# Performance work log

Hardware: AMD Instinct MI355X
Metric: run time of the kernel (lower is better)

Reference implementation:

```python
import jax, jax.numpy as jnp
import numpy as np


def setup_inputs() -> dict:
    key = jax.random.key(0)
    ks = jax.random.split(key, 6)
    B, S, D, E = 4, 2048, 1024, 8
    H = 4 * D
    return {
        "x": jax.random.normal(ks[0], (B, S, D), dtype=jnp.float32),
        "logits": jax.random.normal(ks[1], (B, S, E), dtype=jnp.float32),
        "noise": jax.random.normal(ks[2], (B, S, E), dtype=jnp.float32),
        "W1": jax.random.normal(ks[3], (E, D, H), dtype=jnp.float32) * (1.0 / np.sqrt(D)),
        "b1": jnp.zeros((E, H), dtype=jnp.float32),
        "W2": jax.random.normal(ks[4], (E, H, D), dtype=jnp.float32) * (1.0 / np.sqrt(H)),
        "b2": jnp.zeros((E, D), dtype=jnp.float32),
        "top_k": 2,
    }


def reference(x, logits, noise, W1, b1, W2, b2, top_k):
    # NoisyTopkRouter_Cluster: noise scaled by softplus(logits), then sparse top-k softmax
    B, S, D = x.shape
    E = logits.shape[-1]
    noisy = logits + noise * jax.nn.softplus(logits)           # [B,S,E]
    _, topi = jax.lax.top_k(noisy, top_k)                      # [B,S,K]
    in_topk = jax.nn.one_hot(topi, E, dtype=jnp.bool_).any(-2)  # [B,S,E]
    sparse = jnp.where(in_topk, noisy, -jnp.inf)
    gates = jax.nn.softmax(sparse, axis=-1)                    # [B,S,E]; zero off top-k

    # SparseMoE combine: sum_e gate[:, e] * Expert_e(x). Gate is exactly 0 for
    # unselected experts, so dense-masked compute matches the gather/scatter loop.
    xf = x.reshape(-1, D)                                      # [T,D]
    gf = gates.reshape(-1, E).T                                # [E,T]

    def body(acc, params):
        w1, bb1, w2, bb2, g = params                           # g: [T]
        h = jax.nn.relu(xf @ w1 + bb1)                         # [T,4D]
        acc = acc + (h @ w2 + bb2) * g[:, None]
        return acc, None

    acc, _ = jax.lax.scan(body, jnp.zeros_like(xf), (W1, b1, W2, b2, gf))
    return acc.reshape(B, S, D)
```

## Files before the change

### kernel.cpp

```cpp
#include <hip/hip_runtime.h>
#include <cstdint>
#include <cstddef>

#define T_TOK 8192
#define E_NUM 8
#define D_DIM 1024
#define H_DIM 4096
#define MAXTILES 136
#define TILE 128
#define BK 32

typedef __attribute__((ext_vector_type(8))) short short8;
typedef __attribute__((ext_vector_type(4))) float f32x4;
typedef __attribute__((ext_vector_type(8))) unsigned short ushort8v;
typedef __attribute__((ext_vector_type(4))) unsigned short ushort4v;

__device__ __forceinline__ unsigned short f2b(float f) {
  unsigned int u = __float_as_uint(f);
  u += 0x7fffu + ((u >> 16) & 1u);
  return (unsigned short)(u >> 16);
}

__device__ __forceinline__ void async16(const void* g, void* l) {
  __builtin_amdgcn_global_load_lds((const __attribute__((address_space(1))) void*)g,
                                   (__attribute__((address_space(3))) void*)l, 16, 0, 0);
}

__global__ void router_kernel(const float* __restrict__ logits, const float* __restrict__ noise,
                              int* __restrict__ counts, int* __restrict__ ti, float* __restrict__ tg) {
  int tk = blockIdx.x * blockDim.x + threadIdx.x;
  if (tk >= T_TOK) return;
  float nz[E_NUM];
#pragma unroll
  for (int e = 0; e < E_NUM; ++e) {
    float l = logits[tk * E_NUM + e];
    float sp = fmaxf(l, 0.f) + log1pf(expf(-fabsf(l)));
    nz[e] = l + noise[tk * E_NUM + e] * sp;
  }
  int i1 = 0; float v1 = nz[0];
#pragma unroll
  for (int e = 1; e < E_NUM; ++e) if (nz[e] > v1) { v1 = nz[e]; i1 = e; }
  int i2 = -1; float v2 = -3.0e38f;
#pragma unroll
  for (int e = 0; e < E_NUM; ++e) if (e != i1 && nz[e] > v2) { v2 = nz[e]; i2 = e; }
  float ex = expf(v2 - v1);
  float g1 = 1.f / (1.f + ex);
  float g2 = ex / (1.f + ex);
  int s1 = atomicAdd(&counts[i1], 1);
  int s2 = atomicAdd(&counts[i2], 1);
  ti[tk*4+0] = i1; ti[tk*4+1] = s1; ti[tk*4+2] = i2; ti[tk*4+3] = s2;
  tg[tk*2+0] = g1; tg[tk*2+1] = g2;
}

__global__ void setup_kernel(const int* __restrict__ counts, int* __restrict__ offs,
                             int* __restrict__ tab) {
  int o = 0;
  for (int e = 0; e < E_NUM; ++e) { offs[e] = o; o += counts[e]; }
  offs[E_NUM] = o;
  int mt = 0;
  for (int e = 0; e < E_NUM; ++e)
    for (int m0 = 0; m0 < counts[e]; m0 += TILE) { tab[mt*2] = e; tab[mt*2+1] = m0; ++mt; }
  for (; mt < MAXTILES; ++mt) { tab[mt*2] = -1; tab[mt*2+1] = 0; }
}

__global__ void gather_kernel(const float* __restrict__ x, const int* __restrict__ ti,
                              const float* __restrict__ tg, const int* __restrict__ offs,
                              unsigned short* __restrict__ xg, int* __restrict__ stok,
                              float* __restrict__ sg) {
  const int tk = blockIdx.x, t = threadIdx.x;
  const int i1 = ti[tk*4+0], s1 = ti[tk*4+1], i2 = ti[tk*4+2], s2 = ti[tk*4+3];
  const int r1 = offs[i1] + s1, r2 = offs[i2] + s2;
  if (t == 0) {
    stok[r1] = tk; sg[r1] = tg[tk*2+0];
    stok[r2] = tk; sg[r2] = tg[tk*2+1];
  }
  const float4 v = *(const float4*)(x + (size_t)tk * D_DIM + t * 4);
  ushort4v bb; bb.x = f2b(v.x); bb.y = f2b(v.y); bb.z = f2b(v.z); bb.w = f2b(v.w);
  *(ushort4v*)(xg + (size_t)r1 * D_DIM + t * 4) = bb;
  *(ushort4v*)(xg + (size_t)r2 * D_DIM + t * 4) = bb;
}

__global__ void transpose_kernel(const float* __restrict__ W, unsigned short* __restrict__ Wt,
                                 int K, int N) {
  const int e = blockIdx.z;
  const float* We = W + (size_t)e * K * N;
  unsigned short* Wte = Wt + (size_t)e * K * N;
  __shared__ __align__(16) unsigned short tb[64 * 72];
  const int n0 = blockIdx.x * 64, k0 = blockIdx.y * 64;
  const int t = threadIdx.x;
  const int kr = t >> 4;
  const int c4 = (t & 15) * 4;
#pragma unroll
  for (int rr = 0; rr < 4; ++rr) {
    int k = kr + rr * 16;
    const float4 v = *(const float4*)(We + (size_t)(k0 + k) * N + n0 + c4);
    tb[(c4+0)*72 + k] = f2b(v.x);
    tb[(c4+1)*72 + k] = f2b(v.y);
    tb[(c4+2)*72 + k] = f2b(v.z);
    tb[(c4+3)*72 + k] = f2b(v.w);
  }
  __syncthreads();
  const int n = t >> 2, kq = (t & 3) * 16;
  ushort8v a = *(const ushort8v*)&tb[n*72 + kq];
  ushort8v b = *(const ushort8v*)&tb[n*72 + kq + 8];
  *(ushort8v*)(Wte + (size_t)(n0+n)*K + k0 + kq) = a;
  *(ushort8v*)(Wte + (size_t)(n0+n)*K + k0 + kq + 8) = b;
}

template<int EPI, int NX>
__global__ __launch_bounds__(256)
void gemm_bt(const unsigned short* __restrict__ A, const unsigned short* __restrict__ Bt,
             const int K, const int N,
             const int* __restrict__ counts, const int* __restrict__ offs,
             const int* __restrict__ tab,
             const float* __restrict__ bias,
             unsigned short* __restrict__ Hout,
             float* __restrict__ Out,
             const int* __restrict__ slot_tok, const float* __restrict__ slot_gate) {
  constexpr int G = NX / 8;
  const int bid = blockIdx.x;
  const int c = bid & 7;
  const int s = bid >> 3;
  const int xi = c * G + (s % G);
  const int mt = s / G;

  const int e = tab[mt*2];
  if (e < 0) return;
  const int m0  = tab[mt*2+1];
  const int cnt = counts[e];
  const int seg = offs[e];
  const int n0  = xi * TILE;

  __shared__ __align__(16) short As[TILE*BK];
  __shared__ __align__(16) short Bs[TILE*BK];
  __shared__ int   s_tok[TILE];
  __shared__ float s_g[TILE];

  const int t = threadIdx.x;
  const int lane = t & 63;
  const int wv = t >> 6;
  const int wm = wv & 1, wn = wv >> 1;
  const int fr = lane & 15, fq = lane >> 4;

  if (EPI == 1 && t < TILE) {
    int rl = m0 + t;
    if (rl < cnt) { s_tok[t] = slot_tok[seg + rl]; s_g[t] = slot_gate[seg + rl]; }
    else          { s_tok[t] = 0;                  s_g[t] = 0.f; }
  }

  const unsigned short* Ae = A + (size_t)seg * K;
  const unsigned short* Be = Bt + (size_t)e * N * K + (size_t)n0 * K;

  const int row0 = t >> 2;
  const int kcg  = ((t & 3) ^ (row0 & 3)) * 8;
  int ar0 = m0 + row0;        ar0 = ar0 < cnt ? ar0 : cnt - 1;
  int ar1 = m0 + row0 + 64;   ar1 = ar1 < cnt ? ar1 : cnt - 1;
  const unsigned short* gA0 = Ae + (size_t)ar0 * K + kcg;
  const unsigned short* gA1 = Ae + (size_t)ar1 * K + kcg;
  const unsigned short* gB0 = Be + (size_t)row0 * K + kcg;
  const unsigned short* gB1 = Be + (size_t)(row0 + 64) * K + kcg;
  char* lA0 = (char*)As + wv*1024;
  char* lA1 = (char*)As + 4096 + wv*1024;
  char* lB0 = (char*)Bs + wv*1024;
  char* lB1 = (char*)Bs + 4096 + wv*1024;

  f32x4 acc[4][4];
#pragma unroll
  for (int i = 0; i < 4; ++i)
#pragma unroll
    for (int j = 0; j < 4; ++j) acc[i][j] = (f32x4){0.f, 0.f, 0.f, 0.f};

  for (int k0 = 0; k0 < K; k0 += BK) {
    async16(gA0, lA0); async16(gA1, lA1);
    async16(gB0, lB0); async16(gB1, lB1);
    gA0 += BK; gA1 += BK; gB0 += BK; gB1 += BK;
    asm volatile("s_waitcnt vmcnt(0)" ::: "memory");
    __syncthreads();

    short8 af[4], bf[4];
#pragma unroll
    for (int i = 0; i < 4; ++i) {
      int row = wm*64 + i*16 + fr;
      af[i] = *(const short8*)&As[row*BK + (fq ^ (row & 3))*8];
    }
#pragma unroll
    for (int j = 0; j < 4; ++j) {
      int row = wn*64 + j*16 + fr;
      bf[j] = *(const short8*)&Bs[row*BK + (fq ^ (row & 3))*8];
    }
#pragma unroll
    for (int i = 0; i < 4; ++i)
#pragma unroll
      for (int j = 0; j < 4; ++j)
        acc[i][j] = __builtin_amdgcn_mfma_f32_16x16x32_bf16(af[i], bf[j], acc[i][j], 0, 0, 0);
    __syncthreads();
  }

  if (EPI == 0) {
    const float* be = bias + (size_t)e * N;
#pragma unroll
    for (int j = 0; j < 4; ++j) {
      int col = n0 + wn*64 + j*16 + fr;
      float bv = be[col];
#pragma unroll
      for (int i = 0; i < 4; ++i) {
        int rb = m0 + wm*64 + i*16 + fq*4;
#pragma unroll
        for (int r = 0; r < 4; ++r) {
          int rl = rb + r;
          if (rl < cnt) {
            float v = acc[i][j][r] + bv;
            v = v > 0.f ? v : 0.f;
            Hout[(size_t)(seg + rl) * N + col] = f2b(v);
          }
        }
      }
    }
  } else {
    const float* be = bias + (size_t)e * N;
#pragma unroll
    for (int j = 0; j < 4; ++j) {
      int col = n0 + wn*64 + j*16 + fr;
      float bv = be[col];
#pragma unroll
      for (int i = 0; i < 4; ++i) {
        int rbt = wm*64 + i*16 + fq*4;
#pragma unroll
        for (int r = 0; r < 4; ++r) {
          int rlt = rbt + r;
          if (m0 + rlt < cnt) {
            float v = (acc[i][j][r] + bv) * s_g[rlt];
            unsafeAtomicAdd(Out + (size_t)s_tok[rlt] * N + col, v);
          }
        }
      }
    }
  }
}

extern "C" void kernel_launch(void* const* d_in, const int* in_sizes, int n_in,
                              void* d_out, int out_size, void* d_ws, size_t ws_size,
                              hipStream_t stream) {
  const float* x      = (const float*)d_in[0];
  const float* logits = (const float*)d_in[1];
  const float* noise  = (const float*)d_in[2];
  const float* W1     = (const float*)d_in[3];
  const float* b1     = (const float*)d_in[4];
  const float* W2     = (const float*)d_in[5];
  const float* b2     = (const float*)d_in[6];
  float* out = (float*)d_out;

  char* ws = (char*)d_ws;
  size_t off = 0;
  auto alloc = [&](size_t b) { size_t o = off; off = (off + b + 255) & ~(size_t)255; return o; };
  size_t o_counts = alloc(E_NUM * 4);
  size_t o_offs   = alloc((E_NUM + 1) * 4);
  size_t o_tab    = alloc((size_t)MAXTILES * 2 * 4);
  size_t o_ti     = alloc((size_t)T_TOK * 4 * 4);
  size_t o_tg     = alloc((size_t)T_TOK * 2 * 4);
  size_t o_stok   = alloc((size_t)2 * T_TOK * 4);
  size_t o_sg     = alloc((size_t)2 * T_TOK * 4);
  size_t o_xg     = alloc((size_t)2 * T_TOK * D_DIM * 2);
  size_t o_w1t    = alloc((size_t)E_NUM * D_DIM * H_DIM * 2);
  size_t o_w2t    = alloc((size_t)E_NUM * D_DIM * H_DIM * 2);
  size_t o_h      = alloc((size_t)2 * T_TOK * H_DIM * 2);
  if (off > ws_size) return;

  int*            counts = (int*)(ws + o_counts);
  int*            offsp  = (int*)(ws + o_offs);
  int*            tab    = (int*)(ws + o_tab);
  int*            ti     = (int*)(ws + o_ti);
  float*          tg     = (float*)(ws + o_tg);
  int*            stok   = (int*)(ws + o_stok);
  float*          sg     = (float*)(ws + o_sg);
  unsigned short* xg     = (unsigned short*)(ws + o_xg);
  unsigned short* w1t    = (unsigned short*)(ws + o_w1t);
  unsigned short* w2t    = (unsigned short*)(ws + o_w2t);
  unsigned short* h      = (unsigned short*)(ws + o_h);

  hipMemsetAsync(out, 0, (size_t)out_size * sizeof(float), stream);
  hipMemsetAsync(counts, 0, E_NUM * sizeof(int), stream);

  router_kernel<<<T_TOK / 256, 256, 0, stream>>>(logits, noise, counts, ti, tg);
  setup_kernel<<<1, 1, 0, stream>>>(counts, offsp, tab);
  gather_kernel<<<T_TOK, 256, 0, stream>>>(x, ti, tg, offsp, xg, stok, sg);

  transpose_kernel<<<dim3(H_DIM/64, D_DIM/64, E_NUM), 256, 0, stream>>>(W1, w1t, D_DIM, H_DIM);
  transpose_kernel<<<dim3(D_DIM/64, H_DIM/64, E_NUM), 256, 0, stream>>>(W2, w2t, H_DIM, D_DIM);

  gemm_bt<0, H_DIM/TILE><<<dim3((H_DIM/TILE) * MAXTILES), 256, 0, stream>>>(
      xg, w1t, D_DIM, H_DIM, counts, offsp, tab, b1, h, nullptr, nullptr, nullptr);
  gemm_bt<1, D_DIM/TILE><<<dim3((D_DIM/TILE) * MAXTILES), 256, 0, stream>>>(
      h, w2t, H_DIM, D_DIM, counts, offsp, tab, b2, nullptr, out, stok, sg);
}
```

Measured before the change: 999.4 us.

## Triple-buffer async global-to-LDS loads in expert GEMM main loop

Replaces the single-buffered K loop, which waited for all global-to-LDS loads every iteration, with a three-stage ring of LDS buffers. The loop prefetches future K tiles and waits only until the current stage has landed (vmcnt(8)), so global load latency can overlap with MFMA work. In exchange, shared memory per block grows to 48KB, which may lower occupancy. At the tail the prefetch index is clamped, so the last iterations issue redundant loads.

```diff
diff --git a/kernel.cpp b/kernel.cpp
--- a/kernel.cpp
+++ b/kernel.cpp
@@ -9,6 +9,7 @@
 #define MAXTILES 136
 #define TILE 128
 #define BK 32
+#define STAGES 3
 
 typedef __attribute__((ext_vector_type(8))) short short8;
 typedef __attribute__((ext_vector_type(4))) float f32x4;
@@ -131,8 +132,7 @@
   const int seg = offs[e];
   const int n0  = xi * TILE;
 
-  __shared__ __align__(16) short As[TILE*BK];
-  __shared__ __align__(16) short Bs[TILE*BK];
+  __shared__ __align__(16) short smem[STAGES * 2 * TILE * BK];
   __shared__ int   s_tok[TILE];
   __shared__ float s_g[TILE];
 
@@ -147,6 +147,7 @@
     if (rl < cnt) { s_tok[t] = slot_tok[seg + rl]; s_g[t] = slot_gate[seg + rl]; }
     else          { s_tok[t] = 0;                  s_g[t] = 0.f; }
   }
+  __syncthreads();
 
   const unsigned short* Ae = A + (size_t)seg * K;
   const unsigned short* Be = Bt + (size_t)e * N * K + (size_t)n0 * K;
@@ -155,14 +156,20 @@
   const int kcg  = ((t & 3) ^ (row0 & 3)) * 8;
   int ar0 = m0 + row0;        ar0 = ar0 < cnt ? ar0 : cnt - 1;
   int ar1 = m0 + row0 + 64;   ar1 = ar1 < cnt ? ar1 : cnt - 1;
-  const unsigned short* gA0 = Ae + (size_t)ar0 * K + kcg;
-  const unsigned short* gA1 = Ae + (size_t)ar1 * K + kcg;
-  const unsigned short* gB0 = Be + (size_t)row0 * K + kcg;
-  const unsigned short* gB1 = Be + (size_t)(row0 + 64) * K + kcg;
-  char* lA0 = (char*)As + wv*1024;
-  char* lA1 = (char*)As + 4096 + wv*1024;
-  char* lB0 = (char*)Bs + wv*1024;
-  char* lB1 = (char*)Bs + 4096 + wv*1024;
+  const unsigned short* rA0 = Ae + (size_t)ar0 * K + kcg;
+  const unsigned short* rA1 = Ae + (size_t)ar1 * K + kcg;
+  const unsigned short* rB0 = Be + (size_t)row0 * K + kcg;
+  const unsigned short* rB1 = Be + (size_t)(row0 + 64) * K + kcg;
+  const int ldsOff = wv * 1024;
+
+  auto issue = [&](int koff, int soff) {
+    char* pA = (char*)smem + soff + ldsOff;
+    char* pB = (char*)smem + soff + 8192 + ldsOff;
+    async16(rA0 + koff, pA);
+    async16(rA1 + koff, pA + 4096);
+    async16(rB0 + koff, pB);
+    async16(rB1 + koff, pB + 4096);
+  };
 
   f32x4 acc[4][4];
 #pragma unroll
@@ -170,13 +177,17 @@
 #pragma unroll
     for (int j = 0; j < 4; ++j) acc[i][j] = (f32x4){0.f, 0.f, 0.f, 0.f};
 
+  issue(0 * BK, 0 * 16384);
+  issue(1 * BK, 1 * 16384);
+  issue(2 * BK, 2 * 16384);
+
+  int soff = 0;
   for (int k0 = 0; k0 < K; k0 += BK) {
-    async16(gA0, lA0); async16(gA1, lA1);
-    async16(gB0, lB0); async16(gB1, lB1);
-    gA0 += BK; gA1 += BK; gB0 += BK; gB1 += BK;
-    asm volatile("s_waitcnt vmcnt(0)" ::: "memory");
-    __syncthreads();
-
+    asm volatile("s_waitcnt vmcnt(8)" ::: "memory");
+    asm volatile("s_barrier" ::: "memory");
+
+    const short* As = (const short*)((const char*)smem + soff);
+    const short* Bs = (const short*)((const char*)smem + soff + 8192);
     short8 af[4], bf[4];
 #pragma unroll
     for (int i = 0; i < 4; ++i) {
@@ -193,7 +204,13 @@
 #pragma unroll
       for (int j = 0; j < 4; ++j)
         acc[i][j] = __builtin_amdgcn_mfma_f32_16x16x32_bf16(af[i], bf[j], acc[i][j], 0, 0, 0);
-    __syncthreads();
+
+    asm volatile("s_barrier" ::: "memory");
+
+    int kpre = k0 + STAGES * BK;
+    if (kpre > K - BK) kpre = K - BK;
+    issue(kpre, soff);
+    soff += 16384; if (soff == STAGES * 16384) soff = 0;
   }
 
   if (EPI == 0) {
```

Result: faster. 932.3 us (-6.7%).

## Double-buffer GEMM K-loop with register prefetch instead of direct-to-LDS loads

Applied to the files above, without the earlier changes.

Replaces the synchronous global_load_lds staging, which waited on vmcnt(0) every K step, with a two-deep register prefetch and two LDS buffers. Global loads for upcoming K tiles are issued before the MFMA work on the current tile, so memory latency overlaps compute and only one barrier is needed per step. In exchange it uses more VGPRs for prefetch registers and twice the LDS, which may lower occupancy.

```diff
diff --git a/kernel.cpp b/kernel.cpp
--- a/kernel.cpp
+++ b/kernel.cpp
@@ -9,6 +9,7 @@
 #define MAXTILES 136
 #define TILE 128
 #define BK 32
+#define BUFB 16384
 
 typedef __attribute__((ext_vector_type(8))) short short8;
 typedef __attribute__((ext_vector_type(4))) float f32x4;
@@ -19,11 +20,6 @@
   unsigned int u = __float_as_uint(f);
   u += 0x7fffu + ((u >> 16) & 1u);
   return (unsigned short)(u >> 16);
-}
-
-__device__ __forceinline__ void async16(const void* g, void* l) {
-  __builtin_amdgcn_global_load_lds((const __attribute__((address_space(1))) void*)g,
-                                   (__attribute__((address_space(3))) void*)l, 16, 0, 0);
 }
 
 __global__ void router_kernel(const float* __restrict__ logits, const float* __restrict__ noise,
@@ -131,8 +127,7 @@
   const int seg = offs[e];
   const int n0  = xi * TILE;
 
-  __shared__ __align__(16) short As[TILE*BK];
-  __shared__ __align__(16) short Bs[TILE*BK];
+  __shared__ __align__(16) char smem[2 * BUFB];
   __shared__ int   s_tok[TILE];
   __shared__ float s_g[TILE];
 
@@ -152,17 +147,18 @@
   const unsigned short* Be = Bt + (size_t)e * N * K + (size_t)n0 * K;
 
   const int row0 = t >> 2;
-  const int kcg  = ((t & 3) ^ (row0 & 3)) * 8;
+  const int kch  = (t & 3) * 8;
   int ar0 = m0 + row0;        ar0 = ar0 < cnt ? ar0 : cnt - 1;
   int ar1 = m0 + row0 + 64;   ar1 = ar1 < cnt ? ar1 : cnt - 1;
-  const unsigned short* gA0 = Ae + (size_t)ar0 * K + kcg;
-  const unsigned short* gA1 = Ae + (size_t)ar1 * K + kcg;
-  const unsigned short* gB0 = Be + (size_t)row0 * K + kcg;
-  const unsigned short* gB1 = Be + (size_t)(row0 + 64) * K + kcg;
-  char* lA0 = (char*)As + wv*1024;
-  char* lA1 = (char*)As + 4096 + wv*1024;
-  char* lB0 = (char*)Bs + wv*1024;
-  char* lB1 = (char*)Bs + 4096 + wv*1024;
+  const unsigned short* gA0 = Ae + (size_t)ar0 * K + kch;
+  const unsigned short* gA1 = Ae + (size_t)ar1 * K + kch;
+  const unsigned short* gB0 = Be + (size_t)row0 * K + kch;
+  const unsigned short* gB1 = Be + (size_t)(row0 + 64) * K + kch;
+  const int wA0 = row0 * 64 + (((t & 3) ^ (row0 & 3)) * 16);
+  const int wA1 = wA0 + 64 * 64;
+
+  ushort8v p0a0, p0a1, p0b0, p0b1;
+  ushort8v p1a0, p1a1, p1b0, p1b1;
 
   f32x4 acc[4][4];
 #pragma unroll
@@ -170,30 +166,79 @@
 #pragma unroll
     for (int j = 0; j < 4; ++j) acc[i][j] = (f32x4){0.f, 0.f, 0.f, 0.f};
 
-  for (int k0 = 0; k0 < K; k0 += BK) {
-    async16(gA0, lA0); async16(gA1, lA1);
-    async16(gB0, lB0); async16(gB1, lB1);
-    gA0 += BK; gA1 += BK; gB0 += BK; gB1 += BK;
-    asm volatile("s_waitcnt vmcnt(0)" ::: "memory");
-    __syncthreads();
-
-    short8 af[4], bf[4];
-#pragma unroll
-    for (int i = 0; i < 4; ++i) {
-      int row = wm*64 + i*16 + fr;
-      af[i] = *(const short8*)&As[row*BK + (fq ^ (row & 3))*8];
+  p0a0 = *(const ushort8v*)(gA0);      p0a1 = *(const ushort8v*)(gA1);
+  p0b0 = *(const ushort8v*)(gB0);      p0b1 = *(const ushort8v*)(gB1);
+  p1a0 = *(const ushort8v*)(gA0 + BK); p1a1 = *(const ushort8v*)(gA1 + BK);
+  p1b0 = *(const ushort8v*)(gB0 + BK); p1b1 = *(const ushort8v*)(gB1 + BK);
+  *(ushort8v*)(smem + wA0)        = p0a0;
+  *(ushort8v*)(smem + wA1)        = p0a1;
+  *(ushort8v*)(smem + 8192 + wA0) = p0b0;
+  *(ushort8v*)(smem + 8192 + wA1) = p0b1;
+  __syncthreads();
+
+  for (int k0 = 0; k0 < K; k0 += 2 * BK) {
+    {
+      int kpre = k0 + 2 * BK; if (kpre > K - BK) kpre = K - BK;
+      p0a0 = *(const ushort8v*)(gA0 + kpre); p0a1 = *(const ushort8v*)(gA1 + kpre);
+      p0b0 = *(const ushort8v*)(gB0 + kpre); p0b1 = *(const ushort8v*)(gB1 + kpre);
+
+      const short* As = (const short*)(smem);
+      const short* Bs = (const short*)(smem + 8192);
+      short8 af[4], bf[4];
+#pragma unroll
+      for (int i = 0; i < 4; ++i) {
+        int row = wm*64 + i*16 + fr;
+        af[i] = *(const short8*)&As[row*BK + (fq ^ (row & 3))*8];
+      }
+#pragma unroll
+      for (int j = 0; j < 4; ++j) {
+        int row = wn*64 + j*16 + fr;
+        bf[j] = *(const short8*)&Bs[row*BK + (fq ^ (row & 3))*8];
+      }
+#pragma unroll
+      for (int i = 0; i < 4; ++i)
+#pragma unroll
+        for (int j = 0; j < 4; ++j)
+          acc[i][j] = __builtin_amdgcn_mfma_f32_16x16x32_bf16(af[i], bf[j], acc[i][j], 0, 0, 0);
+
+      *(ushort8v*)(smem + BUFB + wA0)        = p1a0;
+      *(ushort8v*)(smem + BUFB + wA1)        = p1a1;
+      *(ushort8v*)(smem + BUFB + 8192 + wA0) = p1b0;
+      *(ushort8v*)(smem + BUFB + 8192 + wA1) = p1b1;
+      __syncthreads();
     }
-#pragma unroll
-    for (int j = 0; j < 4; ++j) {
-      int row = wn*64 + j*16 + fr;
-      bf[j] = *(const short8*)&Bs[row*BK + (fq ^ (row & 3))*8];
+    {
+      int kpre = k0 + 3 * BK; if (kpre > K - BK) kpre = K - BK;
+      p1a0 = *(const ushort8v*)(gA0 + kpre); p1a1 = *(const ushort8v*)(gA1 + kpre);
+      p1b0 = *(const ushort8v*)(gB0 + kpre); p1b1 = *(const ushort8v*)(gB1 + kpre);
+
+      const short* As = (const short*)(smem + BUFB);
+      const short* Bs = (const short*)(smem + BUFB + 8192);
+      short8 af[4], bf[4];
+#pragma unroll
+      for (int i = 0; i < 4; ++i) {
+        int row = wm*64 + i*16 + fr;
+        af[i] = *(const short8*)&As[row*BK + (fq ^ (row & 3))*8];
+      }
+#pragma unroll
+      for (int j = 0; j < 4; ++j) {
+        int row = wn*64 + j*16 + fr;
+        bf[j] = *(const short8*)&Bs[row*BK + (fq ^ (row & 3))*8];
+      }
+#pragma unroll
+      for (int i = 0; i < 4; ++i)
+#pragma unroll
+        for (int j = 0; j < 4; ++j)
+          acc[i][j] = __builtin_amdgcn_mfma_f32_16x16x32_bf16(af[i], bf[j], acc[i][j], 0, 0, 0);
+
+      if (k0 + 2 * BK < K) {
+        *(ushort8v*)(smem + wA0)        = p0a0;
+        *(ushort8v*)(smem + wA1)        = p0a1;
+        *(ushort8v*)(smem + 8192 + wA0) = p0b0;
+        *(ushort8v*)(smem + 8192 + wA1) = p0b1;
+        __syncthreads();
+      }
     }
-#pragma unroll
-    for (int i = 0; i < 4; ++i)
-#pragma unroll
-      for (int j = 0; j < 4; ++j)
-        acc[i][j] = __builtin_amdgcn_mfma_f32_16x16x32_bf16(af[i], bf[j], acc[i][j], 0, 0, 0);
-    __syncthreads();
   }
 
   if (EPI == 0) {
```

New measurement: 1.110 ms. 1.11x slower.
